# Optimization experiments

Hardware: AMD Instinct MI355X
Metric: run time of the kernel (lower is better)

The kernel has to match this reference:

```python
import jax, jax.numpy as jnp
import numpy as np

N_NODES = 50000
IN_CH = 512
HID = 256
HEADS = 4
N_LAYERS = 2
LN_EPS = 1e-5


def _layer_norm(x, g, b):
    mu = jnp.mean(x, axis=-1, keepdims=True)
    var = jnp.mean((x - mu) ** 2, axis=-1, keepdims=True)
    return (x - mu) * jax.lax.rsqrt(var + LN_EPS) * g + b


def _trans_conv(x, wq, bq, wk, bk, wv, bv):
    # x: [N, HID]; projections -> [N, HEADS, HID]
    N = x.shape[0]
    qs = (x @ wq + bq).reshape(N, HEADS, HID)
    ks = (x @ wk + bk).reshape(N, HEADS, HID)
    vs = (x @ wv + bv).reshape(N, HEADS, HID)
    # NOTE: global Frobenius norm, matching torch.norm(t, p=2)
    qs = qs / jnp.linalg.norm(qs)
    ks = ks / jnp.linalg.norm(ks)
    kvs = jnp.einsum('lhm,lhd->hmd', ks, vs)                 # [H, C, C]
    attn_num = jnp.einsum('nhm,hmd->nhd', qs, kvs) + N * vs  # [N, H, C]
    ks_sum = jnp.sum(ks, axis=0)                             # [H, C]
    denom = jnp.einsum('nhm,hm->nh', qs, ks_sum)[..., None] + N
    return jnp.mean(attn_num / denom, axis=1)                # [N, HID]


def setup_inputs() -> dict:
    key = jax.random.key(0)
    ks = jax.random.split(key, 32)
    s_in = 1.0 / np.sqrt(IN_CH)
    s_h = 1.0 / np.sqrt(HID)
    inp = {
        'x': jax.random.normal(ks[0], (N_NODES, IN_CH), jnp.float32),
        'fc_w': jax.random.uniform(ks[1], (IN_CH, HID), jnp.float32, -s_in, s_in),
        'fc_b': jax.random.uniform(ks[2], (HID,), jnp.float32, -s_in, s_in),
        'ln0_g': jnp.ones((HID,), jnp.float32),
        'ln0_b': jnp.zeros((HID,), jnp.float32),
    }
    for i in range(N_LAYERS):
        base = 3 + i * 8
        inp[f'wq{i}'] = jax.random.uniform(ks[base + 0], (HID, HID * HEADS), jnp.float32, -s_h, s_h)
        inp[f'bq{i}'] = jax.random.uniform(ks[base + 1], (HID * HEADS,), jnp.float32, -s_h, s_h)
        inp[f'wk{i}'] = jax.random.uniform(ks[base + 2], (HID, HID * HEADS), jnp.float32, -s_h, s_h)
        inp[f'bk{i}'] = jax.random.uniform(ks[base + 3], (HID * HEADS,), jnp.float32, -s_h, s_h)
        inp[f'wv{i}'] = jax.random.uniform(ks[base + 4], (HID, HID * HEADS), jnp.float32, -s_h, s_h)
        inp[f'bv{i}'] = jax.random.uniform(ks[base + 5], (HID * HEADS,), jnp.float32, -s_h, s_h)
        inp[f'ln{i + 1}_g'] = jnp.ones((HID,), jnp.float32)
        inp[f'ln{i + 1}_b'] = jnp.zeros((HID,), jnp.float32)
    return inp


def reference(x, fc_w, fc_b, ln0_g, ln0_b,
              wq0, bq0, wk0, bk0, wv0, bv0, ln1_g, ln1_b,
              wq1, bq1, wk1, bk1, wv1, bv1, ln2_g, ln2_b):
    # input FFN path (ffn is hard-coded True); dropout is identity in eval mode
    h = jax.nn.relu(_layer_norm(x @ fc_w + fc_b, ln0_g, ln0_b))
    layers = [(wq0, bq0, wk0, bk0, wv0, bv0, ln1_g, ln1_b),
              (wq1, bq1, wk1, bk1, wv1, bv1, ln2_g, ln2_b)]
    for (wq, bq, wk, bk, wv, bv, g, b) in layers:
        prev = h
        h = _trans_conv(h, wq, bq, wk, bk, wv, bv)
        h = (h + prev) / 2.0
        h = jax.nn.relu(_layer_norm(h, g, b))
    return h
```

## Files before the change

kernel.cpp:

```cpp
#include <hip/hip_runtime.h>

#define NN    50000
#define IN_CH 512
#define HID   256
#define PJ    1024
#define FN    50000.0f
#define KTP   50176
#define NCH   98
#define CHK   512

typedef __attribute__((ext_vector_type(4)))  float f32x4;
typedef __attribute__((ext_vector_type(16))) float f32x16;
typedef __attribute__((ext_vector_type(4)))  int   i32x4;
typedef __attribute__((ext_vector_type(8)))  unsigned short u16x8;

__device__ inline void mfma16(f32x4& c, i32x4 a, i32x4 b){
  asm("v_mfma_f32_16x16x32_bf16 %0, %1, %2, %0" : "+v"(c) : "v"(a), "v"(b));
}
__device__ inline void mfma32(f32x16& c, i32x4 a, i32x4 b){
  asm("v_mfma_f32_32x32x16_bf16 %0, %1, %2, %0" : "+v"(c) : "v"(a), "v"(b));
}

__device__ inline unsigned short f2bf(float f){
  unsigned int u = __builtin_bit_cast(unsigned int, f);
  unsigned int r = (u + 0x7fffu + ((u >> 16) & 1u)) >> 16;
  return (unsigned short)r;
}
__device__ inline float bf2f(unsigned short u){
  unsigned int x = ((unsigned int)u) << 16;
  return __builtin_bit_cast(float, x);
}

__device__ inline float wave_reduce(float v){
  #pragma unroll
  for(int o=32;o>0;o>>=1) v += __shfl_down(v,o,64);
  return v;
}
__device__ inline float block_reduce(float v, float* sh4){
  v = wave_reduce(v);
  int lane = threadIdx.x & 63, wv = threadIdx.x >> 6;
  if(lane==0) sh4[wv] = v;
  __syncthreads();
  float r = sh4[0]+sh4[1]+sh4[2]+sh4[3];
  __syncthreads();
  return r;
}

__global__ void wconv(const float* __restrict__ w, unsigned short* __restrict__ wt){
  int idx = blockIdx.x*256 + threadIdx.x;
  if(idx >= IN_CH*HID) return;
  int k = idx >> 8, n = idx & 255;
  wt[((size_t)(k>>6)*256 + n)*64 + (k&63)] = f2bf(w[idx]);
}

__global__ __launch_bounds__(512)
void ffn_gemm(const float* __restrict__ X, const unsigned short* __restrict__ FWT2,
              const float* __restrict__ bias, const float* __restrict__ g,
              const float* __restrict__ b2, unsigned short* __restrict__ hbo){
  __shared__ __align__(16) unsigned char smem[55296];
  unsigned short (*as)[72] = (unsigned short(*)[72])smem;
  unsigned short (*bs)[72] = (unsigned short(*)[72])(smem + 18432);
  int t = threadIdx.x;
  int bm = blockIdx.x*128;
  int w = t>>6, lane = t&63;
  int wr = w>>2, wc = w&3;
  f32x4 acc[4][4];
  #pragma unroll
  for(int i=0;i<4;i++)
    #pragma unroll
    for(int j=0;j<4;j++) acc[i][j] = (f32x4){0.f,0.f,0.f,0.f};

  for(int k0=0;k0<IN_CH;k0+=64){
    { int r = t>>2, q = t&3;
      const float* src = X + (size_t)(bm+r)*IN_CH + k0 + q*16;
      bool ok = (bm+r) < NN;
      #pragma unroll
      for(int i=0;i<4;i++){
        float4 v = ok ? *(const float4*)(src + i*4) : make_float4(0.f,0.f,0.f,0.f);
        ushort4 u; u.x=f2bf(v.x); u.y=f2bf(v.y); u.z=f2bf(v.z); u.w=f2bf(v.w);
        *(ushort4*)&as[r][q*16 + i*4] = u;
      }
    }
    { int n = t>>1, q = t&1;
      const unsigned short* src = FWT2 + (size_t)(k0>>6)*16384 + (size_t)t*32;
      #pragma unroll
      for(int i=0;i<4;i++)
        *(u16x8*)&bs[n][q*32 + i*8] = *(const u16x8*)(src + i*8);
    }
    __syncthreads();
    #pragma unroll
    for(int ks=0;ks<2;ks++){
      i32x4 af[4], bfv[4];
      #pragma unroll
      for(int i=0;i<4;i++) af[i]  = *(const i32x4*)&as[wr*64 + i*16 + (lane&15)][ks*32 + (lane>>4)*8];
      #pragma unroll
      for(int j=0;j<4;j++) bfv[j] = *(const i32x4*)&bs[wc*64 + j*16 + (lane&15)][ks*32 + (lane>>4)*8];
      #pragma unroll
      for(int i=0;i<4;i++)
        #pragma unroll
        for(int j=0;j<4;j++) mfma16(acc[i][j], af[i], bfv[j]);
    }
    __syncthreads();
  }
  int cb = wc*64;
  #pragma unroll
  for(int j=0;j<4;j++){
    float bb = bias[cb + j*16 + (lane&15)];
    #pragma unroll
    for(int i=0;i<4;i++)
      #pragma unroll
      for(int r=0;r<4;r++) acc[i][j][r] += bb;
  }
  float (*lnp)[4][2] = (float(*)[4][2])smem;
  float (*lnstat)[2] = (float(*)[2])(smem + 4096);
  #pragma unroll
  for(int i=0;i<4;i++)
    #pragma unroll
    for(int r=0;r<4;r++){
      float s=0.f, q=0.f;
      #pragma unroll
      for(int j=0;j<4;j++){ float a=acc[i][j][r]; s+=a; q+=a*a; }
      #pragma unroll
      for(int m=1;m<16;m<<=1){ s += __shfl_xor(s,m,64); q += __shfl_xor(q,m,64); }
      if((lane&15)==0){
        int row = wr*64 + i*16 + (lane>>4)*4 + r;
        lnp[row][wc][0]=s; lnp[row][wc][1]=q;
      }
    }
  __syncthreads();
  if(t<128){
    float s=0.f,q=0.f;
    #pragma unroll
    for(int c=0;c<4;c++){ s+=lnp[t][c][0]; q+=lnp[t][c][1]; }
    float mu = s*(1.f/HID);
    float var = q*(1.f/HID) - mu*mu;
    lnstat[t][0]=mu; lnstat[t][1]=rsqrtf(var+1e-5f);
  }
  __syncthreads();
  #pragma unroll
  for(int j=0;j<4;j++){
    int col = cb + j*16 + (lane&15);
    float gg = g[col], bb = b2[col];
    #pragma unroll
    for(int i=0;i<4;i++)
      #pragma unroll
      for(int r=0;r<4;r++){
        int row = wr*64 + i*16 + (lane>>4)*4 + r;
        int grow = bm + row;
        if(grow<NN){
          float y = fmaxf((acc[i][j][r]-lnstat[row][0])*lnstat[row][1]*gg + bb, 0.f);
          hbo[(size_t)grow*HID + col] = f2bf(y);
        }
      }
  }
}

__global__ void ln_relu2(const float* __restrict__ in, const float* __restrict__ g,
                         const float* __restrict__ b, unsigned short* __restrict__ outb,
                         float* __restrict__ outf, int M){
  int lane = threadIdx.x & 63, wv = threadIdx.x >> 6;
  int row = blockIdx.x*4 + wv;
  if(row>=M) return;
  const float* r = in + (size_t)row*HID;
  float v[4], sum=0.f, sq=0.f;
  #pragma unroll
  for(int j=0;j<4;j++){ v[j]=r[lane+j*64]; sum+=v[j]; sq+=v[j]*v[j]; }
  sum = wave_reduce(sum); sq = wave_reduce(sq);
  sum = __shfl(sum,0,64); sq = __shfl(sq,0,64);
  float mu = sum*(1.f/HID);
  float var = sq*(1.f/HID) - mu*mu;
  float rs = rsqrtf(var + 1e-5f);
  #pragma unroll
  for(int j=0;j<4;j++){ int c=lane+j*64;
    float y = fmaxf((v[j]-mu)*rs*g[c] + b[c], 0.f);
    if(outb) outb[(size_t)row*HID + c] = f2bf(y);
    if(outf) outf[(size_t)row*HID + c] = y;
  }
}

__global__ __launch_bounds__(256)
void transpose_h(const unsigned short* __restrict__ hb, unsigned short* __restrict__ ht){
  __shared__ unsigned short ts[64][72];
  int r0 = blockIdx.x*64, c0 = blockIdx.y*64;
  int t = threadIdx.x;
  { int r = t&63, q = t>>6;
    #pragma unroll
    for(int i=0;i<2;i++){
      int c = q*16 + i*8;
      u16x8 v = {0,0,0,0,0,0,0,0};
      if(r0+r < NN) v = *(const u16x8*)(hb + (size_t)(r0+r)*HID + c0 + c);
      *(u16x8*)&ts[r][c] = v;
    }
  }
  __syncthreads();
  { int c = t>>2, q = t&3;
    unsigned short tmp[16];
    #pragma unroll
    for(int i=0;i<16;i++) tmp[i] = ts[q*16+i][c];
    unsigned short* dst = ht + (size_t)(c0+c)*KTP + r0 + q*16;
    *(u16x8*)(dst)   = *(u16x8*)&tmp[0];
    *(u16x8*)(dst+8) = *(u16x8*)&tmp[8];
  }
}

__global__ __launch_bounds__(256)
void gram_mfma(const unsigned short* __restrict__ ht, float* __restrict__ gp){
  __shared__ unsigned short as[128][72], bs[128][72];
  int q = blockIdx.x, ch = blockIdx.y;
  int r0 = (q>>1)*128, c0 = (q&1)*128;
  int t = threadIdx.x, w=t>>6, lane=t&63;
  int wr=w>>1, wc=w&1;
  f32x4 acc[4][4];
  #pragma unroll
  for(int i=0;i<4;i++)
    #pragma unroll
    for(int j=0;j<4;j++) acc[i][j] = (f32x4){0.f,0.f,0.f,0.f};
  size_t kbase = (size_t)ch*CHK;
  for(int k0=0;k0<CHK;k0+=64){
    { int r = t>>1, h2 = t&1;
      const unsigned short* srcA = ht + (size_t)(r0+r)*KTP + kbase + k0 + h2*32;
      const unsigned short* srcB = ht + (size_t)(c0+r)*KTP + kbase + k0 + h2*32;
      #pragma unroll
      for(int i=0;i<4;i++) *(u16x8*)&as[r][h2*32+i*8] = *(const u16x8*)(srcA + i*8);
      #pragma unroll
      for(int i=0;i<4;i++) *(u16x8*)&bs[r][h2*32+i*8] = *(const u16x8*)(srcB + i*8);
    }
    __syncthreads();
    #pragma unroll
    for(int ks=0;ks<2;ks++){
      i32x4 af[4], bfv[4];
      #pragma unroll
      for(int i=0;i<4;i++) af[i]  = *(const i32x4*)&as[wr*64 + i*16 + (lane&15)][ks*32 + (lane>>4)*8];
      #pragma unroll
      for(int j=0;j<4;j++) bfv[j] = *(const i32x4*)&bs[wc*64 + j*16 + (lane&15)][ks*32 + (lane>>4)*8];
      #pragma unroll
      for(int i=0;i<4;i++)
        #pragma unroll
        for(int j=0;j<4;j++) mfma16(acc[i][j], af[i], bfv[j]);
    }
    __syncthreads();
  }
  float* dst = gp + ((size_t)q*NCH + ch)*16384;
  #pragma unroll
  for(int i=0;i<4;i++)
    #pragma unroll
    for(int j=0;j<4;j++)
      #pragma unroll
      for(int r=0;r<4;r++)
        dst[(wr*64+i*16+(lane>>4)*4+r)*128 + wc*64+j*16+(lane&15)] = acc[i][j][r];
}

__global__ void gram_reduce2(const float* __restrict__ gp, float* __restrict__ G){
  int q=blockIdx.x; int e = blockIdx.y*256 + threadIdx.x;
  const float* p = gp + (size_t)q*NCH*16384 + e;
  float s=0.f;
  for(int c=0;c<NCH;c++) s += p[(size_t)c*16384];
  int i = e>>7, j = e&127;
  int r0=(q>>1)*128, c0=(q&1)*128;
  G[(r0+i)*256 + c0+j] = s;
}

__global__ void rowsum_ht(const unsigned short* __restrict__ ht, float* __restrict__ svec){
  int row = blockIdx.x;
  const unsigned short* p = ht + (size_t)row*KTP;
  float s = 0.f;
  for(int i = threadIdx.x*8; i < KTP; i += 2048){
    u16x8 v = *(const u16x8*)(p + i);
    #pragma unroll
    for(int e=0;e<8;e++) s += bf2f(v[e]);
  }
  __shared__ float sh4[4];
  float tot = block_reduce(s, sh4);
  if(threadIdx.x==0) svec[row] = tot;
}

__global__ void gw_gemm3(const float* __restrict__ G, const float* __restrict__ Wq,
                         const float* __restrict__ Wk, const float* __restrict__ Wv,
                         float* __restrict__ gw){
  const float* B = blockIdx.z==0?Wq:(blockIdx.z==1?Wk:Wv);
  float* C = gw + (size_t)blockIdx.z*262144;
  __shared__ float As[64][33];
  __shared__ float Bs[32][64];
  int bm = blockIdx.x*64, bn = blockIdx.y*64;
  int t = threadIdx.x;
  int tn = t & 15, tm = t >> 4;
  float acc[4][4] = {};
  for(int k0=0;k0<HID;k0+=32){
    { int kk=t&31, rr=t>>5;
      #pragma unroll
      for(int p=0;p<8;p++){ int r=rr+p*8;
        As[r][kk] = G[(size_t)(bm+r)*HID + k0+kk]; } }
    { int nn=t&63, kr=t>>6;
      #pragma unroll
      for(int p=0;p<8;p++){ int k=kr+p*4;
        Bs[k][nn] = B[(size_t)(k0+k)*PJ + bn+nn]; } }
    __syncthreads();
    for(int k=0;k<32;k++){
      float a[4], b[4];
      #pragma unroll
      for(int i=0;i<4;i++) a[i]=As[tm*4+i][k];
      #pragma unroll
      for(int j=0;j<4;j++) b[j]=Bs[k][tn*4+j];
      #pragma unroll
      for(int i=0;i<4;i++)
        #pragma unroll
        for(int j=0;j<4;j++) acc[i][j] += a[i]*b[j];
    }
    __syncthreads();
  }
  #pragma unroll
  for(int i=0;i<4;i++)
    #pragma unroll
    for(int j=0;j<4;j++)
      C[(size_t)(bm+tm*4+i)*PJ + bn+tn*4+j] = acc[i][j];
}

__global__ void wt_s(const float* __restrict__ Wq, const float* __restrict__ Wk,
                     const float* __restrict__ Wv, const float* __restrict__ s,
                     float* __restrict__ avec){
  const float* Wsel = (blockIdx.x==0)?Wq:(blockIdx.x==1)?Wk:Wv;
  int col = blockIdx.y*256 + threadIdx.x;
  __shared__ float ss[256];
  ss[threadIdx.x]=s[threadIdx.x];
  __syncthreads();
  float acc=0.f;
  for(int i=0;i<256;i++) acc += Wsel[(size_t)i*PJ + col]*ss[i];
  avec[blockIdx.x*1024 + col]=acc;
}

__global__ void trace_partial(const float* __restrict__ Wq, const float* __restrict__ Wk,
                              const float* __restrict__ gw, float* __restrict__ trp){
  int which = blockIdx.x;
  const float* Wsel = which ? Wk : Wq;
  const float* GW = gw + (size_t)which*262144;
  int t=threadIdx.x;
  int base = blockIdx.y*4096 + t;
  float s=0.f;
  #pragma unroll
  for(int i=0;i<16;i++){ int idx=base+i*256; s += Wsel[idx]*GW[idx]; }
  __shared__ float sh4[4];
  float r = block_reduce(s, sh4);
  if(t==0) trp[which*64 + blockIdx.y] = r;
}

__global__ void finalize_scalars(const float* __restrict__ trp, const float* __restrict__ bq,
                                 const float* __restrict__ bk, const float* __restrict__ avec,
                                 float* __restrict__ ksum, float* __restrict__ scal){
  __shared__ float sh4[4];
  int t=threadIdx.x;
  float pq = (t<64)? trp[t]    : 0.f;
  float pk = (t<64)? trp[64+t] : 0.f;
  float bqaq=0.f,bkak=0.f,bq2=0.f,bk2=0.f;
  #pragma unroll
  for(int p=0;p<4;p++){ int jn=t+p*256;
    float qv=bq[jn], kv=bk[jn];
    bqaq += qv*avec[jn]; bkak += kv*avec[1024+jn];
    bq2 += qv*qv; bk2 += kv*kv; }
  float tq = block_reduce(pq, sh4);
  float tk = block_reduce(pk, sh4);
  float s1 = block_reduce(bqaq, sh4);
  float s2 = block_reduce(bkak, sh4);
  float s3 = block_reduce(bq2, sh4);
  float s4 = block_reduce(bk2, sh4);
  if(t==0){
    float q2 = tq + 2.f*s1 + FN*s3;
    float k2 = tk + 2.f*s2 + FN*s4;
    scal[0] = rsqrtf(q2)*rsqrtf(k2);
  }
  #pragma unroll
  for(int p=0;p<4;p++){ int jn=t+p*256; ksum[jn] = avec[1024+jn] + FN*bk[jn]; }
}

__global__ void kvs_k(const float* __restrict__ Wk, const float* __restrict__ GWv,
                      const float* __restrict__ avec, const float* __restrict__ bk,
                      const float* __restrict__ bv, float* __restrict__ kvs){
  int hh=blockIdx.x, tile=blockIdx.y;
  int m0=(tile>>2)*64, d0=(tile&3)*64;
  __shared__ float As[32][64], Bs[32][64];
  int t=threadIdx.x, tn=t&15, tm=t>>4;
  float acc[4][4]={};
  for(int k0=0;k0<256;k0+=32){
    int kr=t>>6, cc=t&63;
    #pragma unroll
    for(int p=0;p<8;p++){
      int k=kr+p*4;
      As[k][cc] = Wk [(size_t)(k0+k)*PJ + hh*256 + m0+cc];
      Bs[k][cc] = GWv[(size_t)(k0+k)*PJ + hh*256 + d0+cc];
    }
    __syncthreads();
    for(int k=0;k<32;k++){
      float a[4], b[4];
      #pragma unroll
      for(int i=0;i<4;i++) a[i]=As[k][tm*4+i];
      #pragma unroll
      for(int j=0;j<4;j++) b[j]=Bs[k][tn*4+j];
      #pragma unroll
      for(int i=0;i<4;i++)
        #pragma unroll
        for(int j=0;j<4;j++) acc[i][j] += a[i]*b[j];
    }
    __syncthreads();
  }
  const float* ak = avec+1024; const float* av = avec+2048;
  #pragma unroll
  for(int i=0;i<4;i++)
    #pragma unroll
    for(int j=0;j<4;j++){
      int m=m0+tm*4+i, d=d0+tn*4+j;
      float akm=ak[hh*256+m], bkm=bk[hh*256+m];
      float avd=av[hh*256+d], bvd=bv[hh*256+d];
      kvs[(size_t)hh*65536 + m*256 + d] = acc[i][j] + akm*bvd + bkm*avd + FN*bkm*bvd;
    }
}

__global__ void u_gemm(const float* __restrict__ Wq, const float* __restrict__ kvs,
                       const float* __restrict__ Wv, const float* __restrict__ scal,
                       unsigned short* __restrict__ Ut2){
  int hh=blockIdx.x, tile=blockIdx.y;
  int i0=(tile>>2)*64, d0=(tile&3)*64;
  __shared__ float As[64][33]; __shared__ float Bs[32][64];
  int t=threadIdx.x, tn=t&15, tm=t>>4;
  float acc[4][4]={};
  for(int k0=0;k0<256;k0+=32){
    { int kk=t&31, rr=t>>5;
      #pragma unroll
      for(int p=0;p<8;p++){ int r=rr+p*8;
        As[r][kk] = Wq[(size_t)(i0+r)*PJ + hh*256 + k0+kk]; } }
    { int kr=t>>6, cc=t&63;
      #pragma unroll
      for(int p=0;p<8;p++){ int k=kr+p*4;
        Bs[k][cc] = kvs[(size_t)hh*65536 + (k0+k)*256 + d0+cc]; } }
    __syncthreads();
    for(int k=0;k<32;k++){
      float a[4], b[4];
      #pragma unroll
      for(int i=0;i<4;i++) a[i]=As[tm*4+i][k];
      #pragma unroll
      for(int j=0;j<4;j++) b[j]=Bs[k][tn*4+j];
      #pragma unroll
      for(int i=0;i<4;i++)
        #pragma unroll
        for(int j=0;j<4;j++) acc[i][j] += a[i]*b[j];
    }
    __syncthreads();
  }
  float sc = scal[0];
  #pragma unroll
  for(int i=0;i<4;i++)
    #pragma unroll
    for(int j=0;j<4;j++){
      int ii=i0+tm*4+i, d=d0+tn*4+j;
      float val = sc*acc[i][j] + FN*Wv[(size_t)ii*PJ + hh*256 + d];
      Ut2[((size_t)(d>>6)*4 + (ii>>6))*16384 + ((size_t)hh*64 + (d&63))*64 + (ii&63)] = f2bf(val);
    }
}

__global__ void head_vecs(const float* __restrict__ Wq, const float* __restrict__ bq,
                          const float* __restrict__ bv, const float* __restrict__ kvs,
                          const float* __restrict__ ksum, const float* __restrict__ scal,
                          float* __restrict__ uvec, float* __restrict__ wvec,
                          float* __restrict__ cvec){
  int hh=blockIdx.x, t=threadIdx.x;
  float scale=scal[0];
  __shared__ float bqs[256], kss[256];
  __shared__ float sh4[4];
  bqs[t]=bq[hh*256+t]; kss[t]=ksum[hh*256+t];
  __syncthreads();
  float su=0.f;
  for(int m=0;m<256;m++) su += bqs[m]*kvs[(size_t)hh*65536 + m*256 + t];
  uvec[hh*256+t] = scale*su + FN*bv[hh*256+t];
  float sw=0.f;
  for(int m=0;m<256;m++) sw += Wq[(size_t)t*PJ + hh*256 + m]*kss[m];
  wvec[hh*256+t] = scale*sw;
  float pc = bqs[t]*kss[t];
  float total = block_reduce(pc, sh4);
  if(t==0) cvec[hh] = scale*total + FN;
}

__global__ void denom_k(const unsigned short* __restrict__ hb, const float* __restrict__ wvec,
                        const float* __restrict__ cvec, float* __restrict__ denom, int M){
  __shared__ float wvl[1024];
  for(int i=threadIdx.x;i<1024;i+=256) wvl[i]=wvec[i];
  __syncthreads();
  int lane=threadIdx.x&63, wv=threadIdx.x>>6;
  int row=blockIdx.x*4+wv;
  if(row>=M) return;
  ushort4 hv = *(const ushort4*)(hb + (size_t)row*HID + lane*4);
  float h0=bf2f(hv.x), h1=bf2f(hv.y), h2=bf2f(hv.z), h3=bf2f(hv.w);
  float p[4];
  #pragma unroll
  for(int hh=0;hh<4;hh++){
    const float* wl = wvl + hh*256 + lane*4;
    p[hh] = h0*wl[0] + h1*wl[1] + h2*wl[2] + h3*wl[3];
  }
  #pragma unroll
  for(int hh=0;hh<4;hh++) p[hh]=wave_reduce(p[hh]);
  if(lane==0){
    #pragma unroll
    for(int hh=0;hh<4;hh++) denom[(size_t)row*4+hh] = 1.0f/(p[hh]+cvec[hh]);
  }
}

__global__ __launch_bounds__(512,4)
void attn_mfma(const unsigned short* __restrict__ hb, const unsigned short* __restrict__ Ut2,
               const float* __restrict__ uvec, const float* __restrict__ rden,
               float* __restrict__ outp){
  __shared__ __align__(16) unsigned char smem[38912];
  unsigned short (*bs)[72] = (unsigned short(*)[72])smem;
  float (*red)[64] = (float(*)[64])smem;
  float (*rsh)[4]  = (float(*)[4])(smem + 36864);
  int bm = blockIdx.x*128;
  int st = blockIdx.y;
  int t = threadIdx.x, w = t>>6, lane = t&63;
  int wr = w>>1, wc = w&1;
  int nst = t>>1, koff = (t&1)*32;

  f32x16 acc[4];
  #pragma unroll
  for(int j=0;j<4;j++)
    #pragma unroll
    for(int e=0;e<16;e++) acc[j][e]=0.f;

  { int r = t>>2, h2 = t&3;
    rsh[r][h2] = (bm+r<NN) ? rden[(size_t)(bm+r)*4+h2] : 1.0f; }

  const unsigned short* tb0 = Ut2 + (size_t)st*4*16384;
  u16x8 breg[4];
  #pragma unroll
  for(int i=0;i<4;i++) breg[i] = *(const u16x8*)(tb0 + (size_t)t*32 + i*8);

  int arow = bm + wr*32 + (lane&31); if(arow >= NN) arow = NN-1;
  const unsigned short* ap = hb + (size_t)arow*HID + (lane>>5)*8;

  #pragma unroll
  for(int kb=0;kb<4;kb++){
    __syncthreads();
    #pragma unroll
    for(int i=0;i<4;i++) *(u16x8*)&bs[nst][koff + i*8] = breg[i];
    __syncthreads();
    if(kb<3){
      const unsigned short* tn2 = Ut2 + ((size_t)st*4 + kb+1)*16384;
      #pragma unroll
      for(int i=0;i<4;i++) breg[i] = *(const u16x8*)(tn2 + (size_t)t*32 + i*8);
    }
    i32x4 a[4];
    #pragma unroll
    for(int ks=0;ks<4;ks++) a[ks] = *(const i32x4*)(ap + kb*64 + ks*16);
    #pragma unroll
    for(int ks=0;ks<4;ks++){
      int kc = ks*16 + (lane>>5)*8;
      #pragma unroll
      for(int j=0;j<4;j++){
        i32x4 b = *(const i32x4*)&bs[wc*128 + j*32 + (lane&31)][kc];
        mfma32(acc[j], a[ks], b);
      }
    }
  }
  float uv[4];
  #pragma unroll
  for(int j=0;j<4;j++)
    uv[j] = uvec[(wc*2 + (j>>1))*256 + st*64 + (j&1)*32 + (lane&31)];
  __syncthreads();
  if(wc==1){
    #pragma unroll
    for(int r=0;r<16;r++){
      int row = wr*32 + (r&3) + ((r>>2)<<3) + ((lane>>5)<<2);
      float d0 = rsh[row][2], d1 = rsh[row][3];
      red[row][lane&31]      = (acc[0][r]+uv[0])*d0 + (acc[2][r]+uv[2])*d1;
      red[row][32+(lane&31)] = (acc[1][r]+uv[1])*d0 + (acc[3][r]+uv[3])*d1;
    }
  }
  __syncthreads();
  if(wc==0){
    #pragma unroll
    for(int r=0;r<16;r++){
      int row = wr*32 + (r&3) + ((r>>2)<<3) + ((lane>>5)<<2);
      int gr = bm + row;
      if(gr < NN){
        float d0 = rsh[row][0], d1 = rsh[row][1];
        float v0 = ((acc[0][r]+uv[0])*d0 + (acc[2][r]+uv[2])*d1 + red[row][lane&31])      * 0.25f;
        float v1 = ((acc[1][r]+uv[1])*d0 + (acc[3][r]+uv[3])*d1 + red[row][32+(lane&31)]) * 0.25f;
        const unsigned short* hres = hb + (size_t)gr*HID + st*64;
        float* dst = outp + (size_t)gr*HID + st*64;
        dst[lane&31]      = (v0 + bf2f(hres[lane&31])) * 0.5f;
        dst[32+(lane&31)] = (v1 + bf2f(hres[32+(lane&31)])) * 0.5f;
      }
    }
  }
}

extern "C" void kernel_launch(void* const* d_in, const int* in_sizes, int n_in,
                              void* d_out, int out_size, void* d_ws, size_t ws_size,
                              hipStream_t stream){
  const float* x    = (const float*)d_in[0];
  const float* fc_w = (const float*)d_in[1];
  const float* fc_b = (const float*)d_in[2];
  const float* ln0g = (const float*)d_in[3];
  const float* ln0b = (const float*)d_in[4];
  float* out = (float*)d_out;

  float* W = (float*)d_ws;
  size_t o=0;
  float* buf1 = W+o; o+=(size_t)NN*HID;
  unsigned short* hb   = (unsigned short*)(W+o); o+=(size_t)NN*HID/2;
  unsigned short* ht   = (unsigned short*)(W+o); o+=(size_t)HID*KTP/2;
  unsigned short* FWT2 = (unsigned short*)(W+o); o+=(size_t)8*16384/2 + 8;
  unsigned short* Ut2  = (unsigned short*)(W+o); o+=(size_t)16*16384/2 + 8;
  float* gramp= W+o; o+=(size_t)4*NCH*16384;
  float* G    = W+o; o+=65536;
  float* gw   = W+o; o+=3*262144;
  float* svec = W+o; o+=256;
  float* avec = W+o; o+=3072;
  float* trp  = W+o; o+=128;
  float* scal = W+o; o+=16;
  float* ksum = W+o; o+=1024;
  float* kvs  = W+o; o+=262144;
  float* uvec = W+o; o+=1024;
  float* wvec = W+o; o+=1024;
  float* cvec = W+o; o+=8;
  float* denB = W+o; o+=(size_t)NN*4;
  (void)ws_size; (void)in_sizes; (void)n_in; (void)out_size;

  dim3 blk(256);
  wconv<<<dim3(512),blk,0,stream>>>(fc_w, FWT2);
  ffn_gemm<<<dim3(391),dim3(512),0,stream>>>(x, FWT2, fc_b, ln0g, ln0b, hb);

  for(int L=0; L<2; L++){
    const float* wq = (const float*)d_in[5+L*8+0];
    const float* bq = (const float*)d_in[5+L*8+1];
    const float* wk = (const float*)d_in[5+L*8+2];
    const float* bk = (const float*)d_in[5+L*8+3];
    const float* wv = (const float*)d_in[5+L*8+4];
    const float* bv = (const float*)d_in[5+L*8+5];
    const float* lng= (const float*)d_in[5+L*8+6];
    const float* lnb= (const float*)d_in[5+L*8+7];

    transpose_h<<<dim3(784,4),blk,0,stream>>>(hb, ht);
    gram_mfma<<<dim3(4,NCH),blk,0,stream>>>(ht, gramp);
    gram_reduce2<<<dim3(4,64),blk,0,stream>>>(gramp, G);
    rowsum_ht<<<dim3(256),blk,0,stream>>>(ht, svec);
    gw_gemm3<<<dim3(4,16,3),blk,0,stream>>>(G, wq, wk, wv, gw);
    wt_s<<<dim3(3,4),blk,0,stream>>>(wq,wk,wv,svec,avec);
    trace_partial<<<dim3(2,64),blk,0,stream>>>(wq,wk,gw,trp);
    finalize_scalars<<<dim3(1),blk,0,stream>>>(trp,bq,bk,avec,ksum,scal);
    kvs_k<<<dim3(4,16),blk,0,stream>>>(wk, gw+2*262144, avec, bk, bv, kvs);
    u_gemm<<<dim3(4,16),blk,0,stream>>>(wq, kvs, wv, scal, Ut2);
    head_vecs<<<dim3(4),blk,0,stream>>>(wq,bq,bv,kvs,ksum,scal,uvec,wvec,cvec);
    denom_k<<<dim3(12500),blk,0,stream>>>(hb, wvec, cvec, denB, NN);
    attn_mfma<<<dim3(391,4),dim3(512),0,stream>>>(hb, Ut2, uvec, denB, buf1);
    ln_relu2<<<dim3(12500),blk,0,stream>>>(buf1, lng, lnb,
                                           L ? (unsigned short*)nullptr : hb,
                                           L ? out : (float*)nullptr, NN);
  }
}
```

Before: 520.0 us.

## Retile FFN GEMM with 32x32 MFMA, exploit Gram symmetry, fuse small kernels

The FFN GEMM now runs 64-row tiles with 256 threads and 32x32x16 MFMA instructions. Next-tile global loads are prefetched into registers so they overlap compute. The Gram-matrix computation skips the redundant lower-left quadrant because the matrix is symmetric, and the reduction mirrors that block into place. The wt_s and trace_partial kernels are folded into gw_gemm3, which removes two launches and re-reads of the weights and gw. The trade-off is extra register pressure in the FFN kernel and more complex epilogue logic in gw_gemm3.

New measurement: 690.1 us. 32.7% more time.

```diff
diff --git a/kernel.cpp b/kernel.cpp
--- a/kernel.cpp
+++ b/kernel.cpp
@@ -53,82 +53,94 @@
   wt[((size_t)(k>>6)*256 + n)*64 + (k&63)] = f2bf(w[idx]);
 }
 
-__global__ __launch_bounds__(512)
+__global__ __launch_bounds__(256,3)
 void ffn_gemm(const float* __restrict__ X, const unsigned short* __restrict__ FWT2,
               const float* __restrict__ bias, const float* __restrict__ g,
               const float* __restrict__ b2, unsigned short* __restrict__ hbo){
-  __shared__ __align__(16) unsigned char smem[55296];
+  __shared__ __align__(16) unsigned char smem[46080];
   unsigned short (*as)[72] = (unsigned short(*)[72])smem;
-  unsigned short (*bs)[72] = (unsigned short(*)[72])(smem + 18432);
+  unsigned short (*bs)[72] = (unsigned short(*)[72])(smem + 9216);
+  float (*lnp)[4][2] = (float(*)[4][2])smem;
+  float (*lnstat)[2] = (float(*)[2])(smem + 2048);
   int t = threadIdx.x;
-  int bm = blockIdx.x*128;
+  int bm = blockIdx.x*64;
   int w = t>>6, lane = t&63;
-  int wr = w>>2, wc = w&3;
-  f32x4 acc[4][4];
-  #pragma unroll
-  for(int i=0;i<4;i++)
-    #pragma unroll
-    for(int j=0;j<4;j++) acc[i][j] = (f32x4){0.f,0.f,0.f,0.f};
-
-  for(int k0=0;k0<IN_CH;k0+=64){
-    { int r = t>>2, q = t&3;
-      const float* src = X + (size_t)(bm+r)*IN_CH + k0 + q*16;
-      bool ok = (bm+r) < NN;
+  f32x16 acc[2][2];
+  #pragma unroll
+  for(int i=0;i<2;i++)
+    #pragma unroll
+    for(int j=0;j<2;j++)
+      #pragma unroll
+      for(int e=0;e<16;e++) acc[i][j][e]=0.f;
+
+  int ar = t>>2, aq = t&3;
+  bool aok = (bm+ar) < NN;
+  const float* xsrc = X + (size_t)(bm+ar)*IN_CH + aq*16;
+  ushort4 aregs[4];
+  u16x8 bregs[8];
+  #pragma unroll
+  for(int i=0;i<4;i++){
+    float4 v = aok ? *(const float4*)(xsrc + i*4) : make_float4(0.f,0.f,0.f,0.f);
+    ushort4 u; u.x=f2bf(v.x); u.y=f2bf(v.y); u.z=f2bf(v.z); u.w=f2bf(v.w);
+    aregs[i]=u;
+  }
+  #pragma unroll
+  for(int i=0;i<8;i++) bregs[i] = *(const u16x8*)(FWT2 + (size_t)t*64 + i*8);
+
+  for(int kb=0;kb<8;kb++){
+    __syncthreads();
+    #pragma unroll
+    for(int i=0;i<4;i++) *(ushort4*)&as[ar][aq*16 + i*4] = aregs[i];
+    #pragma unroll
+    for(int i=0;i<8;i++) *(u16x8*)&bs[t][i*8] = bregs[i];
+    __syncthreads();
+    if(kb<7){
+      const float* xs2 = xsrc + (kb+1)*64;
       #pragma unroll
       for(int i=0;i<4;i++){
-        float4 v = ok ? *(const float4*)(src + i*4) : make_float4(0.f,0.f,0.f,0.f);
+        float4 v = aok ? *(const float4*)(xs2 + i*4) : make_float4(0.f,0.f,0.f,0.f);
         ushort4 u; u.x=f2bf(v.x); u.y=f2bf(v.y); u.z=f2bf(v.z); u.w=f2bf(v.w);
-        *(ushort4*)&as[r][q*16 + i*4] = u;
+        aregs[i]=u;
       }
-    }
-    { int n = t>>1, q = t&1;
-      const unsigned short* src = FWT2 + (size_t)(k0>>6)*16384 + (size_t)t*32;
-      #pragma unroll
-      for(int i=0;i<4;i++)
-        *(u16x8*)&bs[n][q*32 + i*8] = *(const u16x8*)(src + i*8);
-    }
-    __syncthreads();
-    #pragma unroll
-    for(int ks=0;ks<2;ks++){
-      i32x4 af[4], bfv[4];
-      #pragma unroll
-      for(int i=0;i<4;i++) af[i]  = *(const i32x4*)&as[wr*64 + i*16 + (lane&15)][ks*32 + (lane>>4)*8];
-      #pragma unroll
-      for(int j=0;j<4;j++) bfv[j] = *(const i32x4*)&bs[wc*64 + j*16 + (lane&15)][ks*32 + (lane>>4)*8];
-      #pragma unroll
-      for(int i=0;i<4;i++)
-        #pragma unroll
-        for(int j=0;j<4;j++) mfma16(acc[i][j], af[i], bfv[j]);
-    }
-    __syncthreads();
-  }
-  int cb = wc*64;
-  #pragma unroll
-  for(int j=0;j<4;j++){
-    float bb = bias[cb + j*16 + (lane&15)];
-    #pragma unroll
-    for(int i=0;i<4;i++)
-      #pragma unroll
-      for(int r=0;r<4;r++) acc[i][j][r] += bb;
-  }
-  float (*lnp)[4][2] = (float(*)[4][2])smem;
-  float (*lnstat)[2] = (float(*)[2])(smem + 4096);
-  #pragma unroll
-  for(int i=0;i<4;i++)
-    #pragma unroll
-    for(int r=0;r<4;r++){
-      float s=0.f, q=0.f;
-      #pragma unroll
-      for(int j=0;j<4;j++){ float a=acc[i][j][r]; s+=a; q+=a*a; }
-      #pragma unroll
-      for(int m=1;m<16;m<<=1){ s += __shfl_xor(s,m,64); q += __shfl_xor(q,m,64); }
-      if((lane&15)==0){
-        int row = wr*64 + i*16 + (lane>>4)*4 + r;
-        lnp[row][wc][0]=s; lnp[row][wc][1]=q;
+      const unsigned short* bsrc = FWT2 + (size_t)(kb+1)*16384 + (size_t)t*64;
+      #pragma unroll
+      for(int i=0;i<8;i++) bregs[i] = *(const u16x8*)(bsrc + i*8);
+    }
+    #pragma unroll
+    for(int ks=0;ks<4;ks++){
+      int kc = ks*16 + (lane>>5)*8;
+      i32x4 a0 = *(const i32x4*)&as[(lane&31)][kc];
+      i32x4 a1 = *(const i32x4*)&as[32+(lane&31)][kc];
+      i32x4 b0 = *(const i32x4*)&bs[w*64 +      (lane&31)][kc];
+      i32x4 b1 = *(const i32x4*)&bs[w*64 + 32 + (lane&31)][kc];
+      mfma32(acc[0][0], a0, b0); mfma32(acc[0][1], a0, b1);
+      mfma32(acc[1][0], a1, b0); mfma32(acc[1][1], a1, b1);
+    }
+  }
+  __syncthreads();
+  #pragma unroll
+  for(int j=0;j<2;j++){
+    float bb = bias[w*64 + j*32 + (lane&31)];
+    #pragma unroll
+    for(int i=0;i<2;i++)
+      #pragma unroll
+      for(int r=0;r<16;r++) acc[i][j][r] += bb;
+  }
+  #pragma unroll
+  for(int i=0;i<2;i++)
+    #pragma unroll
+    for(int r=0;r<16;r++){
+      float s = acc[i][0][r] + acc[i][1][r];
+      float q = acc[i][0][r]*acc[i][0][r] + acc[i][1][r]*acc[i][1][r];
+      #pragma unroll
+      for(int m=1;m<32;m<<=1){ s += __shfl_xor(s,m,64); q += __shfl_xor(q,m,64); }
+      if((lane&31)==0){
+        int row = i*32 + (r&3) + ((r>>2)<<3) + ((lane>>5)<<2);
+        lnp[row][w][0]=s; lnp[row][w][1]=q;
       }
     }
   __syncthreads();
-  if(t<128){
+  if(t<64){
     float s=0.f,q=0.f;
     #pragma unroll
     for(int c=0;c<4;c++){ s+=lnp[t][c][0]; q+=lnp[t][c][1]; }
@@ -138,14 +150,14 @@
   }
   __syncthreads();
   #pragma unroll
-  for(int j=0;j<4;j++){
-    int col = cb + j*16 + (lane&15);
+  for(int j=0;j<2;j++){
+    int col = w*64 + j*32 + (lane&31);
     float gg = g[col], bb = b2[col];
     #pragma unroll
-    for(int i=0;i<4;i++)
-      #pragma unroll
-      for(int r=0;r<4;r++){
-        int row = wr*64 + i*16 + (lane>>4)*4 + r;
+    for(int i=0;i<2;i++)
+      #pragma unroll
+      for(int r=0;r<16;r++){
+        int row = i*32 + (r&3) + ((r>>2)<<3) + ((lane>>5)<<2);
         int grow = bm + row;
         if(grow<NN){
           float y = fmaxf((acc[i][j][r]-lnstat[row][0])*lnstat[row][1]*gg + bb, 0.f);
@@ -205,8 +217,9 @@
 
 __global__ __launch_bounds__(256)
 void gram_mfma(const unsigned short* __restrict__ ht, float* __restrict__ gp){
+  const int qmap[3] = {0,1,3};
+  int qi = blockIdx.x, q = qmap[qi], ch = blockIdx.y;
   __shared__ unsigned short as[128][72], bs[128][72];
-  int q = blockIdx.x, ch = blockIdx.y;
   int r0 = (q>>1)*128, c0 = (q&1)*128;
   int t = threadIdx.x, w=t>>6, lane=t&63;
   int wr=w>>1, wc=w&1;
@@ -240,7 +253,7 @@
     }
     __syncthreads();
   }
-  float* dst = gp + ((size_t)q*NCH + ch)*16384;
+  float* dst = gp + ((size_t)qi*NCH + ch)*16384;
   #pragma unroll
   for(int i=0;i<4;i++)
     #pragma unroll
@@ -251,13 +264,14 @@
 }
 
 __global__ void gram_reduce2(const float* __restrict__ gp, float* __restrict__ G){
-  int q=blockIdx.x; int e = blockIdx.y*256 + threadIdx.x;
-  const float* p = gp + (size_t)q*NCH*16384 + e;
+  int qi=blockIdx.x; int e = blockIdx.y*256 + threadIdx.x;
+  const float* p = gp + (size_t)qi*NCH*16384 + e;
   float s=0.f;
   for(int c=0;c<NCH;c++) s += p[(size_t)c*16384];
   int i = e>>7, j = e&127;
-  int r0=(q>>1)*128, c0=(q&1)*128;
+  int r0 = (qi==2)?128:0, c0 = (qi==0)?0:128;
   G[(r0+i)*256 + c0+j] = s;
+  if(qi==1) G[(c0+j)*256 + (r0+i)] = s;
 }
 
 __global__ void rowsum_ht(const unsigned short* __restrict__ ht, float* __restrict__ svec){
@@ -276,15 +290,23 @@
 
 __global__ void gw_gemm3(const float* __restrict__ G, const float* __restrict__ Wq,
                          const float* __restrict__ Wk, const float* __restrict__ Wv,
-                         float* __restrict__ gw){
-  const float* B = blockIdx.z==0?Wq:(blockIdx.z==1?Wk:Wv);
-  float* C = gw + (size_t)blockIdx.z*262144;
+                         const float* __restrict__ svec, float* __restrict__ gw,
+                         float* __restrict__ avec, float* __restrict__ trp){
+  int z = blockIdx.z;
+  const float* B = z==0?Wq:(z==1?Wk:Wv);
+  float* C = gw + (size_t)z*262144;
   __shared__ float As[64][33];
   __shared__ float Bs[32][64];
+  __shared__ float ssv[256];
+  __shared__ float sred[4][64];
+  __shared__ float sh4[4];
   int bm = blockIdx.x*64, bn = blockIdx.y*64;
   int t = threadIdx.x;
   int tn = t & 15, tm = t >> 4;
+  ssv[t] = svec[t];
   float acc[4][4] = {};
+  float sacc = 0.f;
+  int snn = t&63, skq = t>>6;
   for(int k0=0;k0<HID;k0+=32){
     { int kk=t&31, rr=t>>5;
       #pragma unroll
@@ -306,6 +328,10 @@
         #pragma unroll
         for(int j=0;j<4;j++) acc[i][j] += a[i]*b[j];
     }
+    if(bm==0){
+      #pragma unroll
+      for(int kk=0;kk<8;kk++) sacc += ssv[k0 + skq*8 + kk]*Bs[skq*8+kk][snn];
+    }
     __syncthreads();
   }
   #pragma unroll
@@ -313,34 +339,21 @@
     #pragma unroll
     for(int j=0;j<4;j++)
       C[(size_t)(bm+tm*4+i)*PJ + bn+tn*4+j] = acc[i][j];
-}
-
-__global__ void wt_s(const float* __restrict__ Wq, const float* __restrict__ Wk,
-                     const float* __restrict__ Wv, const float* __restrict__ s,
-                     float* __restrict__ avec){
-  const float* Wsel = (blockIdx.x==0)?Wq:(blockIdx.x==1)?Wk:Wv;
-  int col = blockIdx.y*256 + threadIdx.x;
-  __shared__ float ss[256];
-  ss[threadIdx.x]=s[threadIdx.x];
-  __syncthreads();
-  float acc=0.f;
-  for(int i=0;i<256;i++) acc += Wsel[(size_t)i*PJ + col]*ss[i];
-  avec[blockIdx.x*1024 + col]=acc;
-}
-
-__global__ void trace_partial(const float* __restrict__ Wq, const float* __restrict__ Wk,
-                              const float* __restrict__ gw, float* __restrict__ trp){
-  int which = blockIdx.x;
-  const float* Wsel = which ? Wk : Wq;
-  const float* GW = gw + (size_t)which*262144;
-  int t=threadIdx.x;
-  int base = blockIdx.y*4096 + t;
-  float s=0.f;
-  #pragma unroll
-  for(int i=0;i<16;i++){ int idx=base+i*256; s += Wsel[idx]*GW[idx]; }
-  __shared__ float sh4[4];
-  float r = block_reduce(s, sh4);
-  if(t==0) trp[which*64 + blockIdx.y] = r;
+  if(z<2){
+    float tp=0.f;
+    #pragma unroll
+    for(int i=0;i<4;i++)
+      #pragma unroll
+      for(int j=0;j<4;j++)
+        tp += acc[i][j] * B[(size_t)(bm+tm*4+i)*PJ + bn+tn*4+j];
+    float tot = block_reduce(tp, sh4);
+    if(t==0) trp[z*64 + blockIdx.x*16 + blockIdx.y] = tot;
+  }
+  if(bm==0){
+    sred[skq][snn] = sacc;
+    __syncthreads();
+    if(t<64) avec[(size_t)z*1024 + bn + t] = sred[0][t]+sred[1][t]+sred[2][t]+sred[3][t];
+  }
 }
 
 __global__ void finalize_scalars(const float* __restrict__ trp, const float* __restrict__ bq,
@@ -606,7 +619,7 @@
   unsigned short* ht   = (unsigned short*)(W+o); o+=(size_t)HID*KTP/2;
   unsigned short* FWT2 = (unsigned short*)(W+o); o+=(size_t)8*16384/2 + 8;
   unsigned short* Ut2  = (unsigned short*)(W+o); o+=(size_t)16*16384/2 + 8;
-  float* gramp= W+o; o+=(size_t)4*NCH*16384;
+  float* gramp= W+o; o+=(size_t)3*NCH*16384;
   float* G    = W+o; o+=65536;
   float* gw   = W+o; o+=3*262144;
   float* svec = W+o; o+=256;
@@ -623,7 +636,7 @@
 
   dim3 blk(256);
   wconv<<<dim3(512),blk,0,stream>>>(fc_w, FWT2);
-  ffn_gemm<<<dim3(391),dim3(512),0,stream>>>(x, FWT2, fc_b, ln0g, ln0b, hb);
+  ffn_gemm<<<dim3(782),blk,0,stream>>>(x, FWT2, fc_b, ln0g, ln0b, hb);
 
   for(int L=0; L<2; L++){
     const float* wq = (const float*)d_in[5+L*8+0];
@@ -636,12 +649,10 @@
     const float* lnb= (const float*)d_in[5+L*8+7];
 
     transpose_h<<<dim3(784,4),blk,0,stream>>>(hb, ht);
-    gram_mfma<<<dim3(4,NCH),blk,0,stream>>>(ht, gramp);
-    gram_reduce2<<<dim3(4,64),blk,0,stream>>>(gramp, G);
+    gram_mfma<<<dim3(3,NCH),blk,0,stream>>>(ht, gramp);
+    gram_reduce2<<<dim3(3,64),blk,0,stream>>>(gramp, G);
     rowsum_ht<<<dim3(256),blk,0,stream>>>(ht, svec);
-    gw_gemm3<<<dim3(4,16,3),blk,0,stream>>>(G, wq, wk, wv, gw);
-    wt_s<<<dim3(3,4),blk,0,stream>>>(wq,wk,wv,svec,avec);
-    trace_partial<<<dim3(2,64),blk,0,stream>>>(wq,wk,gw,trp);
+    gw_gemm3<<<dim3(4,16,3),blk,0,stream>>>(G, wq, wk, wv, svec, gw, avec, trp);
     finalize_scalars<<<dim3(1),blk,0,stream>>>(trp,bq,bk,avec,ksum,scal);
     kvs_k<<<dim3(4,16),blk,0,stream>>>(wk, gw+2*262144, avec, bk, bv, kvs);
     u_gemm<<<dim3(4,16),blk,0,stream>>>(wq, kvs, wv, scal, Ut2);
```
